# Kernel tuning notes

Measured on AMD Instinct MI355X. Metric: run time of the kernel, lower is better.

The kernel has to match this reference:

```python
import jax, jax.numpy as jnp
import numpy as np

DIM, N_HEADS, N_KV_HEADS = 2048, 32, 8
HEAD_DIM = DIM // N_HEADS            # 64
KV_REPEAT = N_HEADS // N_KV_HEADS    # 4
ROPE_THETA = 10000.0


def _rope(x, start_pos):
    # x: [B, T, Hx, hd]  (rotate-half / GPT-NeoX style RoPE)
    B, T, Hx, hd = x.shape
    half = hd // 2
    inv_freq = 1.0 / (ROPE_THETA ** (jnp.arange(half, dtype=jnp.float32) / half))
    pos = (start_pos + jnp.arange(T)).astype(jnp.float32)
    ang = pos[:, None] * inv_freq[None, :]            # [T, half]
    cos = jnp.cos(ang)[None, :, None, :]              # [1, T, 1, half]
    sin = jnp.sin(ang)[None, :, None, :]
    x1, x2 = x[..., :half], x[..., half:]
    return jnp.concatenate([x1 * cos - x2 * sin, x1 * sin + x2 * cos], axis=-1).astype(x.dtype)


def setup_inputs() -> dict:
    key = jax.random.key(0)
    ks = jax.random.split(key, 5)
    B, T = 2, 2048
    s = 1.0 / np.sqrt(DIM)
    return {
        "x": jax.random.normal(ks[0], (B, T, DIM), dtype=jnp.float32),
        "Wq": jax.random.normal(ks[1], (DIM, N_HEADS * HEAD_DIM), dtype=jnp.float32) * s,
        "Wk": jax.random.normal(ks[2], (DIM, N_KV_HEADS * HEAD_DIM), dtype=jnp.float32) * s,
        "Wv": jax.random.normal(ks[3], (DIM, N_KV_HEADS * HEAD_DIM), dtype=jnp.float32) * s,
        "Wo": jax.random.normal(ks[4], (DIM, DIM), dtype=jnp.float32) * s,
        "start_pos": 0,
    }


def reference(x, Wq, Wk, Wv, Wo, start_pos):
    B, T, _ = x.shape
    G, R, hd = N_KV_HEADS, KV_REPEAT, HEAD_DIM
    # projections -> [B, T, H, hd]
    Q = (x @ Wq).reshape(B, T, N_HEADS, hd)
    K = (x @ Wk).reshape(B, T, G, hd)
    V = (x @ Wv).reshape(B, T, G, hd)
    Q = _rope(Q, start_pos)
    K = _rope(K, start_pos)
    # GQA: group query heads as (G kv-groups, R repeats) matching repeat_interleave order
    Qg = Q.reshape(B, T, G, R, hd)
    scale = 1.0 / jnp.sqrt(jnp.asarray(hd, dtype=Q.dtype))
    scores = jnp.einsum('bqgrd,bkgd->bgrqk', Qg, K) * scale   # [B,G,R,T,T]
    # causal mask (is_causal=True since T > 1)
    causal = jnp.tril(jnp.ones((T, T), dtype=bool))
    scores = jnp.where(causal[None, None, None, :, :], scores, jnp.finfo(scores.dtype).min)
    attn = jax.nn.softmax(scores, axis=-1)
    out = jnp.einsum('bgrqk,bkgd->bqgrd', attn, V).reshape(B, T, DIM)
    y = out @ Wo
    # original also returns (K, V) with heads-first layout [B, G, T, hd]
    return (y, K.transpose(0, 2, 1, 3), V.transpose(0, 2, 1, 3))
```

## Files before the change

kernel.cpp:

```cpp
#include <hip/hip_runtime.h>
#include <hip/hip_bf16.h>
#include <stdint.h>


typedef __attribute__((ext_vector_type(4))) float f32x4;
typedef __attribute__((ext_vector_type(16))) float f32x16;
typedef __attribute__((ext_vector_type(8))) short sfrag;
typedef __attribute__((ext_vector_type(8))) __bf16 bfrag;
typedef __attribute__((ext_vector_type(4))) unsigned int u32x4;
typedef unsigned short u16;

__device__ __forceinline__ f32x4 mfma16(sfrag a, sfrag b, f32x4 c) {
  return __builtin_amdgcn_mfma_f32_16x16x32_bf16(
      __builtin_bit_cast(bfrag, a), __builtin_bit_cast(bfrag, b), c, 0, 0, 0);
}
__device__ __forceinline__ f32x16 mfma32(sfrag a, sfrag b, f32x16 c) {
  return __builtin_amdgcn_mfma_f32_32x32x16_bf16(
      __builtin_bit_cast(bfrag, a), __builtin_bit_cast(bfrag, b), c, 0, 0, 0);
}
__device__ __forceinline__ u16 f2b(float f) {
  return __builtin_bit_cast(u16, (__bf16)f);
}
__device__ __forceinline__ unsigned pack2(float a, float b) {
  return (unsigned)f2b(a) | ((unsigned)f2b(b) << 16);
}
__device__ __forceinline__ void swap32(unsigned& a, unsigned& b) {
  asm("v_permlane32_swap_b32 %0, %1" : "+v"(a), "+v"(b));
}

#define GAS __attribute__((address_space(1)))
#define LAS __attribute__((address_space(3)))
__device__ __forceinline__ void gll16(const void* g, void* l) {
  __builtin_amdgcn_global_load_lds((GAS unsigned int*)g, (LAS unsigned int*)l, 16, 0, 0);
}

__global__ __launch_bounds__(256) void k_convx(const float* __restrict__ X,
                                               u16* __restrict__ Y,
                                               const int* __restrict__ sp,
                                               float2* __restrict__ csn) {
  const int bid = blockIdx.x;
  if (bid < 8192) {
    const int i = (bid * 256 + threadIdx.x) * 4;
    float4 v = *(const float4*)(X + i);
    *(ushort4*)(Y + i) = make_ushort4(f2b(v.x), f2b(v.y), f2b(v.z), f2b(v.w));
  } else {
    const int i = (bid - 8192) * 256 + threadIdx.x;
    const int t = i >> 5, j = i & 31;
    const float freq = powf(10000.0f, -(float)j * (1.0f / 32.0f));
    const float ang = (float)(sp[0] + t) * freq;
    csn[i] = make_float2(cosf(ang), sinf(ang));
  }
}

__global__ __launch_bounds__(256) void k_convTall(const float* __restrict__ Wq,
                                                  const float* __restrict__ Wk,
                                                  const float* __restrict__ Wv,
                                                  const float* __restrict__ Wo,
                                                  u16* __restrict__ Wqkvt,
                                                  u16* __restrict__ Wot) {
  __shared__ float tile[64][65];
  const int bx = blockIdx.x;
  const int k0 = blockIdx.y * 64;
  const float* W; int N, n0; u16* Dst; int nd;
  if (bx < 32)      { W = Wq; N = 2048; n0 = bx * 64;        Dst = Wqkvt; nd = n0; }
  else if (bx < 40) { W = Wk; N = 512;  n0 = (bx - 32) * 64; Dst = Wqkvt; nd = 2048 + n0; }
  else if (bx < 48) { W = Wv; N = 512;  n0 = (bx - 40) * 64; Dst = Wqkvt; nd = 2560 + n0; }
  else              { W = Wo; N = 2048; n0 = (bx - 48) * 64; Dst = Wot;   nd = n0; }
  const int tid = threadIdx.x;
  #pragma unroll
  for (int it = 0; it < 4; ++it) {
    const int idx = it * 256 + tid;
    const int kk = idx >> 4, nq = idx & 15;
    float4 v = *(const float4*)(W + (size_t)(k0 + kk) * N + n0 + nq * 4);
    tile[kk][nq * 4 + 0] = v.x;
    tile[kk][nq * 4 + 1] = v.y;
    tile[kk][nq * 4 + 2] = v.z;
    tile[kk][nq * 4 + 3] = v.w;
  }
  __syncthreads();
  #pragma unroll
  for (int it = 0; it < 4; ++it) {
    const int idx = it * 256 + tid;
    const int nn = idx >> 4, kq = idx & 15;
    ushort4 o;
    o.x = f2b(tile[kq * 4 + 0][nn]);
    o.y = f2b(tile[kq * 4 + 1][nn]);
    o.z = f2b(tile[kq * 4 + 2][nn]);
    o.w = f2b(tile[kq * 4 + 3][nn]);
    *(ushort4*)(Dst + (size_t)(nd + nn) * 2048 + k0 + kq * 4) = o;
  }
}

template<int MODE>
__global__ __launch_bounds__(256, 3) void k_gemm128(const u16* __restrict__ A,
                                                    const u16* __restrict__ Bt,
                                                    float* __restrict__ C,
                                                    int N, int K, int GY,
                                                    const float2* __restrict__ csn,
                                                    u16* __restrict__ Qb,
                                                    u16* __restrict__ Kb,
                                                    float* __restrict__ Kout,
                                                    float* __restrict__ Vout) {
  __shared__ u16 lds[16384];
  char* const L = (char*)&lds[0];
  const int tid = threadIdx.x;
  const int q8 = gridDim.x >> 3;
  const int id2 = (blockIdx.x & 7) * q8 + (blockIdx.x >> 3);
  const int by = id2 % GY, bx = id2 / GY;
  const int wid = tid >> 6, lane = tid & 63;
  const int wm = wid >> 1, wn = wid & 1;
  const int l16 = lane & 15, l4 = lane >> 4;
  const size_t K2 = (size_t)K * 2;
  const char* Ab = (const char*)(A + (size_t)(by * 128) * K);
  const char* Bb = (const char*)(Bt + (size_t)(bx * 128) * K);
  const int NT = K >> 6;

  auto stage = [&](const char* gb, int reg, int t) {
    #pragma unroll
    for (int ld = 0; ld < 4; ++ld) {
      const int p = ld * 4096 + tid * 16;
      const int r = p >> 7;
      const int cb = (p & 127) ^ ((r & 7) << 4);
      gll16(gb + (size_t)r * K2 + (size_t)t * 128 + cb, L + reg + p);
    }
  };

  const int swz = (l16 & 7) << 4;
  const int c0 = (l4 * 16) ^ swz;
  const int c1 = (64 + l4 * 16) ^ swz;
  const int aOff = (wm * 64 + l16) * 128;
  const int bOff = 16384 + (wn * 64 + l16) * 128;

  f32x4 acc[4][4];
  #pragma unroll
  for (int m = 0; m < 4; ++m)
    #pragma unroll
    for (int n = 0; n < 4; ++n) acc[m][n] = f32x4{0.f, 0.f, 0.f, 0.f};

  for (int t = 0; t < NT; ++t) {
    stage(Ab, 0, t);
    stage(Bb, 16384, t);
    __syncthreads();
    sfrag a0[4], a1[4], b0[4], b1[4];
    #pragma unroll
    for (int m = 0; m < 4; ++m) {
      a0[m] = *(const sfrag*)(L + aOff + m * 2048 + c0);
      a1[m] = *(const sfrag*)(L + aOff + m * 2048 + c1);
    }
    #pragma unroll
    for (int n = 0; n < 4; ++n) {
      b0[n] = *(const sfrag*)(L + bOff + n * 2048 + c0);
      b1[n] = *(const sfrag*)(L + bOff + n * 2048 + c1);
    }
    #pragma unroll
    for (int m = 0; m < 4; ++m)
      #pragma unroll
      for (int n = 0; n < 4; ++n) {
        acc[m][n] = mfma16(a0[m], b0[n], acc[m][n]);
        acc[m][n] = mfma16(a1[m], b1[n], acc[m][n]);
      }
    __syncthreads();
  }

  if constexpr (MODE == 0) {
    float* Cb = C + (size_t)(by * 128 + wm * 64) * N + bx * 128 + wn * 64;
    #pragma unroll
    for (int m = 0; m < 4; ++m)
      #pragma unroll
      for (int n = 0; n < 4; ++n)
        #pragma unroll
        for (int r = 0; r < 4; ++r)
          Cb[(size_t)(m * 16 + l4 * 4 + r) * N + n * 16 + l16] = acc[m][n][r];
  } else {
    const int head = bx * 2 + wn;
    const int row0 = by * 128 + wm * 64;
    if (head < 40) {
      u16* Lw = (u16*)(L + wid * 8192);
      const float QS = 0.125f * 1.44269504f;
      const bool isQ = head < 32;
      #pragma unroll
      for (int m = 0; m < 4; ++m)
        #pragma unroll
        for (int r = 0; r < 4; ++r) {
          const int tl = m * 16 + l4 * 4 + r;
          const int tg = row0 + tl;
          const int b = tg >> 11, t = tg & 2047;
          #pragma unroll
          for (int n = 0; n < 2; ++n) {
            const int j = n * 16 + l16;
            const float2 cz = csn[t * 32 + j];
            const float x1 = acc[m][n][r], x2 = acc[m][n + 2][r];
            const float o1 = x1 * cz.x - x2 * cz.y;
            const float o2 = x1 * cz.y + x2 * cz.x;
            if (isQ) {
              Lw[tl * 64 + j]      = f2b(o1 * QS);
              Lw[tl * 64 + j + 32] = f2b(o2 * QS);
            } else {
              Lw[tl * 64 + j]      = f2b(o1);
              Lw[tl * 64 + j + 32] = f2b(o2);
              const int g = head - 32;
              const size_t o = (((size_t)b * 8 + g) * 2048 + t) * 64 + j;
              Kout[o] = o1;  Kout[o + 32] = o2;
            }
          }
        }
      __syncthreads();
      u16* dst = isQ ? Qb : Kb;
      const int hh = isQ ? head : (head - 32);
      const int hstride = isQ ? 32 : 8;
      #pragma unroll
      for (int it = 0; it < 8; ++it) {
        const int tl = it * 8 + (lane >> 3);
        const int col = (lane & 7) * 8;
        const u32x4 v = *(const u32x4*)&Lw[tl * 64 + col];
        const int tg = row0 + tl;
        const int b = tg >> 11, t = tg & 2047;
        *(u32x4*)(dst + (((size_t)b * hstride + hh) * 2048 + t) * 64 + col) = v;
      }
    } else {
      const int g = head - 40;
      #pragma unroll
      for (int m = 0; m < 4; ++m)
        #pragma unroll
        for (int r = 0; r < 4; ++r) {
          const int tg = row0 + m * 16 + l4 * 4 + r;
          const int b = tg >> 11, t = tg & 2047;
          const size_t o = (((size_t)b * 8 + g) * 2048 + t) * 64;
          #pragma unroll
          for (int n = 0; n < 4; ++n)
            Vout[o + n * 16 + l16] = acc[m][n][r];
        }
    }
  }
}

__global__ __launch_bounds__(256) void k_vtrans(const float* __restrict__ Vout,
                                                u16* __restrict__ Vt) {
  __shared__ float tile[64][65];
  int t0 = blockIdx.x * 64;
  int bg = blockIdx.y;
  const float* src = Vout + (size_t)bg * (2048 * 64);
  #pragma unroll
  for (int p = 0; p < 16; ++p) {
    int idx = p * 256 + threadIdx.x;
    int tt = idx >> 6, d = idx & 63;
    tile[tt][d] = src[(size_t)(t0 + tt) * 64 + d];
  }
  __syncthreads();
  #pragma unroll
  for (int p = 0; p < 16; ++p) {
    int idx = p * 256 + threadIdx.x;
    int d = idx >> 6, tt = idx & 63;
    Vt[((size_t)bg * 64 + d) * 2048 + t0 + tt] = f2b(tile[tt][d]);
  }
}

__device__ __forceinline__ void pv4(const float* p, sfrag v0a, sfrag v0b,
                                    sfrag v1a, sfrag v1b,
                                    f32x16& O0, f32x16& O1, float& l) {
  unsigned w[8];
  #pragma unroll
  for (int j = 0; j < 8; ++j) w[j] = pack2(p[2 * j], p[2 * j + 1]);
  swap32(w[0], w[2]);
  swap32(w[1], w[3]);
  swap32(w[4], w[6]);
  swap32(w[5], w[7]);
  const sfrag pf0 = __builtin_bit_cast(sfrag, u32x4{w[0], w[1], w[2], w[3]});
  const sfrag pf1 = __builtin_bit_cast(sfrag, u32x4{w[4], w[5], w[6], w[7]});
  O0 = mfma32(v0a, pf0, O0);
  O0 = mfma32(v0b, pf1, O0);
  O1 = mfma32(v1a, pf0, O1);
  O1 = mfma32(v1b, pf1, O1);
  float s[8];
  #pragma unroll
  for (int j = 0; j < 8; ++j) s[j] = p[j] + p[j + 8];
  #pragma unroll
  for (int j = 0; j < 4; ++j) s[j] = s[j] + s[j + 4];
  l += (s[0] + s[1]) + (s[2] + s[3]);
}

__device__ __forceinline__ void tile64_l(const u16* __restrict__ buf,
                                         const sfrag* qf, int hi, int l31, int swz,
                                         f32x16& O0, f32x16& O1, float& l) {
  const char* Kl = (const char*)buf;
  const char* Vl = Kl + 8192;
  const int rb = l31 * 128;
  f32x16 Sa = {}, Sb = {};
  #pragma unroll
  for (int ks = 0; ks < 4; ++ks) {
    const int col = (hi * 16 + ks * 32) ^ swz;
    const sfrag ka = *(const sfrag*)(Kl + rb + col);
    const sfrag kb = *(const sfrag*)(Kl + rb + col + 4096);
    Sa = mfma32(ka, qf[ks], Sa);
    Sb = mfma32(kb, qf[ks], Sb);
  }
  float pa[16], pb[16];
  #pragma unroll
  for (int r = 0; r < 16; ++r) {
    pa[r] = __builtin_amdgcn_exp2f(Sa[r]);
    pb[r] = __builtin_amdgcn_exp2f(Sb[r]);
  }
  sfrag v0[4], v1[4];
  #pragma unroll
  for (int s = 0; s < 4; ++s) {
    const int col = (s * 32 + hi * 16) ^ swz;
    v0[s] = *(const sfrag*)(Vl + rb + col);
    v1[s] = *(const sfrag*)(Vl + rb + col + 4096);
  }
  pv4(pa, v0[0], v0[1], v1[0], v1[1], O0, O1, l);
  pv4(pb, v0[2], v0[3], v1[2], v1[3], O0, O1, l);
}

template<bool MASKED>
__device__ __forceinline__ void tile32_l(const u16* __restrict__ buf, int c,
                                         const sfrag* qf, int hi, int l31, int swz,
                                         f32x16& O0, f32x16& O1, float& l) {
  const char* Kl = (const char*)buf;
  const char* Vl = Kl + 8192;
  const int rb = l31 * 128;
  f32x16 S = {};
  #pragma unroll
  for (int ks = 0; ks < 4; ++ks) {
    const int col = (hi * 16 + ks * 32) ^ swz;
    const sfrag k = *(const sfrag*)(Kl + c * 4096 + rb + col);
    S = mfma32(k, qf[ks], S);
  }
  float p[16];
  #pragma unroll
  for (int r = 0; r < 16; ++r) {
    float s = S[r];
    if (MASKED) {
      int kvo = (r & 3) + 8 * (r >> 2) + 4 * hi;
      if (kvo > l31) s = -__builtin_inff();
    }
    p[r] = __builtin_amdgcn_exp2f(s);
  }
  const int colA = (c * 64 + hi * 16) ^ swz;
  const int colB = (c * 64 + 32 + hi * 16) ^ swz;
  const sfrag v0a = *(const sfrag*)(Vl + rb + colA);
  const sfrag v0b = *(const sfrag*)(Vl + rb + colB);
  const sfrag v1a = *(const sfrag*)(Vl + rb + colA + 4096);
  const sfrag v1b = *(const sfrag*)(Vl + rb + colB + 4096);
  pv4(p, v0a, v0b, v1a, v1b, O0, O1, l);
}

__global__ __launch_bounds__(256, 4) void k_attn5(const u16* __restrict__ Qb,
                                                  const u16* __restrict__ Kb,
                                                  const u16* __restrict__ Vt,
                                                  u16* __restrict__ attOut) {
  __shared__ u16 lds[2][8192];
  const int bid = blockIdx.x;
  const int qb = 63 - (bid >> 4);
  const int bg = bid & 15;
  const int b = bg >> 3, g = bg & 7;
  const int wave = threadIdx.x >> 6, lane = threadIdx.x & 63;
  const int h = g * 4 + wave;
  const int hi = lane >> 5, l31 = lane & 31;
  const int qrow0 = qb * 32;
  const int swz = (l31 & 7) << 4;

  const u16* Qp = Qb + (((size_t)b * 32 + h) * 2048 + qrow0 + l31) * 64 + hi * 8;
  sfrag qf[4];
  #pragma unroll
  for (int ks = 0; ks < 4; ++ks) qf[ks] = *(const sfrag*)(Qp + ks * 16);

  const char* Kg = (const char*)(Kb + ((size_t)b * 8 + g) * (2048 * 64));
  const char* Vg = (const char*)(Vt + ((size_t)b * 8 + g) * (64 * 2048));

  auto stage = [&](int bufi, int t) {
    const char* Ktile = Kg + (size_t)t * 8192;
    const char* Vtile = Vg + t * 128;
    #pragma unroll
    for (int rd = 0; rd < 2; ++rd) {
      const int p = rd * 4096 + threadIdx.x * 16;
      const int d = p >> 7;
      const int cb = (p & 127) ^ ((d & 7) << 4);
      const int lbase = rd * 4096 + wave * 1024;
      gll16(Ktile + d * 128 + cb, (char*)&lds[bufi][0] + lbase);
      gll16(Vtile + (size_t)d * 4096 + cb, (char*)&lds[bufi][0] + 8192 + lbase);
    }
  };

  f32x16 O0 = {}, O1 = {};
  float lsum = 0.f;
  const int nfull = qrow0 >> 6;
  int cur = 0;
  stage(0, 0);
  for (int t = 0; t < nfull; ++t) {
    __syncthreads();
    stage(cur ^ 1, t + 1);
    tile64_l(lds[cur], qf, hi, l31, swz, O0, O1, lsum);
    cur ^= 1;
  }
  __syncthreads();
  if (qb & 1) {
    tile32_l<false>(lds[cur], 0, qf, hi, l31, swz, O0, O1, lsum);
    tile32_l<true>(lds[cur], 1, qf, hi, l31, swz, O0, O1, lsum);
  } else {
    tile32_l<true>(lds[cur], 0, qf, hi, l31, swz, O0, O1, lsum);
  }

  const float ltot = lsum + __shfl_xor(lsum, 32);
  const float inv = 1.0f / ltot;
  const size_t orow = ((size_t)b * 2048 + qrow0 + l31) * 2048 + h * 64;
  #pragma unroll
  for (int dt = 0; dt < 2; ++dt) {
    const f32x16& O = dt ? O1 : O0;
    #pragma unroll
    for (int k = 0; k < 4; ++k) {
      ushort4 o;
      o.x = f2b(O[4 * k + 0] * inv);
      o.y = f2b(O[4 * k + 1] * inv);
      o.z = f2b(O[4 * k + 2] * inv);
      o.w = f2b(O[4 * k + 3] * inv);
      *(ushort4*)&attOut[orow + dt * 32 + 8 * k + 4 * hi] = o;
    }
  }
}

extern "C" void kernel_launch(void* const* d_in, const int* in_sizes, int n_in,
                              void* d_out, int out_size, void* d_ws, size_t ws_size,
                              hipStream_t stream) {
  const float* x  = (const float*)d_in[0];
  const float* Wq = (const float*)d_in[1];
  const float* Wk = (const float*)d_in[2];
  const float* Wv = (const float*)d_in[3];
  const float* Wo = (const float*)d_in[4];
  const int* sp   = (const int*)d_in[5];
  float* y    = (float*)d_out;
  float* Kout = y + 8388608;
  float* Vout = y + 10485760;

  char* ws = (char*)d_ws;
  u16*    xb     = (u16*)(ws + 0);
  u16*    Wqkvt  = (u16*)(ws + 16777216);
  u16*    Wot    = (u16*)(ws + 29360128);
  float2* csn    = (float2*)(ws + 37748736);
  u16*    Qbuf   = (u16*)(ws + 88080384);
  u16*    Kbuf   = (u16*)(ws + 104857600);
  u16*    Vt     = (u16*)(ws + 109051904);
  u16*    attOut = xb;

  k_convx<<<8448, 256, 0, stream>>>(x, xb, sp, csn);
  k_convTall<<<dim3(80, 32), 256, 0, stream>>>(Wq, Wk, Wv, Wo, Wqkvt, Wot);
  k_gemm128<1><<<768, 256, 0, stream>>>(xb, Wqkvt, nullptr, 3072, 2048, 32,
                                        csn, Qbuf, Kbuf, Kout, Vout);
  k_vtrans<<<dim3(32, 16), 256, 0, stream>>>(Vout, Vt);
  k_attn5<<<1024, 256, 0, stream>>>(Qbuf, Kbuf, Vt, attOut);
  k_gemm128<0><<<512, 256, 0, stream>>>(attOut, Wot, y, 2048, 2048, 32,
                                        nullptr, nullptr, nullptr, nullptr, nullptr);
}
```

Before: 184.9 us.

## Process two 32-row query blocks per wave to reuse staged K/V tiles

The attention kernel now gives each wave 64 query rows (two 32-row sub-blocks) instead of 32. Each K/V tile staged into LDS is used by both sub-blocks, which halves the global-to-LDS traffic and the barriers per unit of work. The grid drops from 1024 to 512 blocks. The extra accumulators raise register pressure, so launch bounds go from 4 to 2 blocks per CU, giving lower occupancy and coarser load balance across the causal triangle.

```diff
diff --git a/kernel.cpp b/kernel.cpp
--- a/kernel.cpp
+++ b/kernel.cpp
@@ -344,25 +344,28 @@
   pv4(p, v0a, v0b, v1a, v1b, O0, O1, l);
 }
 
-__global__ __launch_bounds__(256, 4) void k_attn5(const u16* __restrict__ Qb,
+__global__ __launch_bounds__(256, 2) void k_attn7(const u16* __restrict__ Qb,
                                                   const u16* __restrict__ Kb,
                                                   const u16* __restrict__ Vt,
                                                   u16* __restrict__ attOut) {
   __shared__ u16 lds[2][8192];
   const int bid = blockIdx.x;
-  const int qb = 63 - (bid >> 4);
+  const int qb2 = 31 - (bid >> 4);
   const int bg = bid & 15;
   const int b = bg >> 3, g = bg & 7;
   const int wave = threadIdx.x >> 6, lane = threadIdx.x & 63;
   const int h = g * 4 + wave;
   const int hi = lane >> 5, l31 = lane & 31;
-  const int qrow0 = qb * 32;
+  const int qrow0 = qb2 * 64;
   const int swz = (l31 & 7) << 4;
 
-  const u16* Qp = Qb + (((size_t)b * 32 + h) * 2048 + qrow0 + l31) * 64 + hi * 8;
-  sfrag qf[4];
-  #pragma unroll
-  for (int ks = 0; ks < 4; ++ks) qf[ks] = *(const sfrag*)(Qp + ks * 16);
+  const u16* Qp0 = Qb + (((size_t)b * 32 + h) * 2048 + qrow0 + l31) * 64 + hi * 8;
+  sfrag qf0[4], qf1[4];
+  #pragma unroll
+  for (int ks = 0; ks < 4; ++ks) {
+    qf0[ks] = *(const sfrag*)(Qp0 + ks * 16);
+    qf1[ks] = *(const sfrag*)(Qp0 + 32 * 64 + ks * 16);
+  }
 
   const char* Kg = (const char*)(Kb + ((size_t)b * 8 + g) * (2048 * 64));
   const char* Vg = (const char*)(Vt + ((size_t)b * 8 + g) * (64 * 2048));
@@ -381,39 +384,41 @@
     }
   };
 
-  f32x16 O0 = {}, O1 = {};
-  float lsum = 0.f;
-  const int nfull = qrow0 >> 6;
+  f32x16 O00 = {}, O01 = {}, O10 = {}, O11 = {};
+  float ls0 = 0.f, ls1 = 0.f;
+  const int nfull = qb2;
   int cur = 0;
   stage(0, 0);
   for (int t = 0; t < nfull; ++t) {
     __syncthreads();
     stage(cur ^ 1, t + 1);
-    tile64_l(lds[cur], qf, hi, l31, swz, O0, O1, lsum);
+    tile64_l(lds[cur], qf0, hi, l31, swz, O00, O01, ls0);
+    tile64_l(lds[cur], qf1, hi, l31, swz, O10, O11, ls1);
     cur ^= 1;
   }
   __syncthreads();
-  if (qb & 1) {
-    tile32_l<false>(lds[cur], 0, qf, hi, l31, swz, O0, O1, lsum);
-    tile32_l<true>(lds[cur], 1, qf, hi, l31, swz, O0, O1, lsum);
-  } else {
-    tile32_l<true>(lds[cur], 0, qf, hi, l31, swz, O0, O1, lsum);
-  }
-
-  const float ltot = lsum + __shfl_xor(lsum, 32);
-  const float inv = 1.0f / ltot;
-  const size_t orow = ((size_t)b * 2048 + qrow0 + l31) * 2048 + h * 64;
-  #pragma unroll
-  for (int dt = 0; dt < 2; ++dt) {
-    const f32x16& O = dt ? O1 : O0;
-    #pragma unroll
-    for (int k = 0; k < 4; ++k) {
-      ushort4 o;
-      o.x = f2b(O[4 * k + 0] * inv);
-      o.y = f2b(O[4 * k + 1] * inv);
-      o.z = f2b(O[4 * k + 2] * inv);
-      o.w = f2b(O[4 * k + 3] * inv);
-      *(ushort4*)&attOut[orow + dt * 32 + 8 * k + 4 * hi] = o;
+  tile32_l<true >(lds[cur], 0, qf0, hi, l31, swz, O00, O01, ls0);
+  tile32_l<false>(lds[cur], 0, qf1, hi, l31, swz, O10, O11, ls1);
+  tile32_l<true >(lds[cur], 1, qf1, hi, l31, swz, O10, O11, ls1);
+
+  #pragma unroll
+  for (int sb = 0; sb < 2; ++sb) {
+    const float lsum = sb ? ls1 : ls0;
+    const float ltot = lsum + __shfl_xor(lsum, 32);
+    const float inv = 1.0f / ltot;
+    const size_t orow = ((size_t)b * 2048 + qrow0 + sb * 32 + l31) * 2048 + h * 64;
+    #pragma unroll
+    for (int dt = 0; dt < 2; ++dt) {
+      const f32x16& O = sb ? (dt ? O11 : O10) : (dt ? O01 : O00);
+      #pragma unroll
+      for (int k = 0; k < 4; ++k) {
+        ushort4 o;
+        o.x = f2b(O[4 * k + 0] * inv);
+        o.y = f2b(O[4 * k + 1] * inv);
+        o.z = f2b(O[4 * k + 2] * inv);
+        o.w = f2b(O[4 * k + 3] * inv);
+        *(ushort4*)&attOut[orow + dt * 32 + 8 * k + 4 * hi] = o;
+      }
     }
   }
 }
@@ -446,7 +451,7 @@
   k_gemm128<1><<<768, 256, 0, stream>>>(xb, Wqkvt, nullptr, 3072, 2048, 32,
                                         csn, Qbuf, Kbuf, Kout, Vout);
   k_vtrans<<<dim3(32, 16), 256, 0, stream>>>(Vout, Vt);
-  k_attn5<<<1024, 256, 0, stream>>>(Qbuf, Kbuf, Vt, attOut);
+  k_attn7<<<512, 256, 0, stream>>>(Qbuf, Kbuf, Vt, attOut);
   k_gemm128<0><<<512, 256, 0, stream>>>(attOut, Wot, y, 2048, 2048, 32,
                                         nullptr, nullptr, nullptr, nullptr, nullptr);
 }
```

Result: no change. 184.2 us (-0.4%).
